# Optimization experiments

Measured on AMD Instinct MI355X. Metric: run time of the kernel, lower is better.

The kernel has to match this reference:

```python
import jax, jax.numpy as jnp
import numpy as np


def _gather_masked(seq, mask, k):
    """Order-preserving gather of the k True positions per row (apply_mask).
    mask rows are constructed to have exactly k ones, so pad_sequence is a no-op."""
    # stable argsort of ~mask puts True-position indices first, in original order
    idx = jnp.argsort(jnp.logical_not(mask), axis=1, stable=True)[:, :k]  # (B, k)
    return jnp.take_along_axis(seq, idx[:, :, None], axis=1)  # (B, k, H)


def setup_inputs() -> dict:
    B, L, H, K = 8, 4096, 1024, 512
    key = jax.random.key(0)
    k1, k2, k3 = jax.random.split(key, 3)
    sequence_output = jax.random.normal(k1, (B, L, H), dtype=jnp.float32)
    # masks: exactly K source and K target positions per sample (disjoint)
    rng = np.random.default_rng(0)
    src_mask = np.zeros((B, L), dtype=bool)
    tgt_mask = np.zeros((B, L), dtype=bool)
    for i in range(B):
        perm = rng.permutation(L)
        src_mask[i, perm[:K]] = True
        tgt_mask[i, perm[K:2 * K]] = True
    weight = jax.random.normal(k2, (2 * H,), dtype=jnp.float32) * 0.02  # classifier Linear(2H -> 1)
    bias = jax.random.normal(k3, (1,), dtype=jnp.float32) * 0.02
    return {
        "sequence_output": sequence_output,
        "source_mask": jnp.asarray(src_mask),
        "target_mask": jnp.asarray(tgt_mask),
        "weight": weight,
        "bias": bias,
        "num_tokens": K,
    }


def reference(sequence_output, source_mask, target_mask, weight, bias, num_tokens):
    B, L, H = sequence_output.shape
    K = num_tokens  # S == T == K (required by the original expand())
    src = _gather_masked(sequence_output, source_mask, K)  # (B, K, H)
    tgt = _gather_masked(sequence_output, target_mask, K)  # (B, K, H)
    # Original: cat([src.unsqueeze(2).expand(B,S,T,H), tgt.unsqueeze(2).expand(B,S,T,H)])
    # -> combined[b,s,t] = [src[b,s], tgt[b,s]]  (target indexed by s, faithful to source)
    # Decompose Linear(2H,1) on the broadcast-concat: col[b,s] = src@w1 + tgt@w2 + b,
    # then broadcast over t. Same math, no (B,S,T,2H) intermediate.
    col = src @ weight[:H] + tgt @ weight[H:] + bias[0]  # (B, K)
    return jnp.broadcast_to(col[:, :, None], (B, K, K))  # logits (B, S, T)
```

## Files before the change

### kernel.cpp

```cpp
#include <hip/hip_runtime.h>
#include <hip/hip_bf16.h>


#define L_DIM 4096
#define H_DIM 1024
#define K_DIM 512
#define B_DIM 8

__global__ __launch_bounds__(64) void compact_kernel(
    const void* __restrict__ src_mask, const void* __restrict__ tgt_mask,
    int* __restrict__ src_idx, int* __restrict__ tgt_idx)
{
    const int w = blockIdx.x;
    const int lane = threadIdx.x;
    const int b = w >> 1;
    const unsigned char* mp = (const unsigned char*)((w & 1) ? tgt_mask : src_mask);
    int* op = ((w & 1) ? tgt_idx : src_idx) + b * K_DIM;

    unsigned long long m = 0ull;
    {
        const uint4* pb = (const uint4*)(mp + (size_t)b * L_DIM);
#pragma unroll
        for (int j = 0; j < 4; ++j) {
            uint4 u = pb[lane * 4 + j];
            const unsigned vals[4] = {u.x, u.y, u.z, u.w};
#pragma unroll
            for (int k = 0; k < 4; ++k) {
                const unsigned v = vals[k];
                const int base = j * 16 + k * 4;
                if (v & 0x000000FFu) m |= 1ull << (base + 0);
                if (v & 0x0000FF00u) m |= 1ull << (base + 1);
                if (v & 0x00FF0000u) m |= 1ull << (base + 2);
                if (v & 0xFF000000u) m |= 1ull << (base + 3);
            }
        }
    }
    int cnt = __popcll(m);
    int tot = cnt;
#pragma unroll
    for (int off = 32; off; off >>= 1) tot += __shfl_xor(tot, off, 64);

    if (tot != K_DIM) {
        m = 0ull;
        const uint4* pi = (const uint4*)((const unsigned*)mp + (size_t)b * L_DIM);
#pragma unroll
        for (int j = 0; j < 16; ++j) {
            uint4 u = pi[lane * 16 + j];
            const int base = j * 4;
            if (u.x) m |= 1ull << (base + 0);
            if (u.y) m |= 1ull << (base + 1);
            if (u.z) m |= 1ull << (base + 2);
            if (u.w) m |= 1ull << (base + 3);
        }
        cnt = __popcll(m);
    }

    int x = cnt;
#pragma unroll
    for (int off = 1; off < 64; off <<= 1) {
        int y = __shfl_up(x, off, 64);
        if (lane >= off) x += y;
    }
    int rank = x - cnt;

    const int basepos = lane * 64;
    while (m) {
        const int j = __builtin_ctzll(m);
        m &= m - 1;
        op[rank++] = basepos + j;
    }
}

__global__ __launch_bounds__(256) void col_bcast_kernel(
    const float* __restrict__ seq, const float* __restrict__ weight,
    const float* __restrict__ bias,
    const int* __restrict__ src_idx, const int* __restrict__ tgt_idx,
    float* __restrict__ out)
{
    const int wave = (blockIdx.x * 256 + threadIdx.x) >> 6;
    const int lane = threadIdx.x & 63;
    const int b = wave >> 9;

    const int ls = src_idx[wave];
    const int lt = tgt_idx[wave];

    const float4* __restrict__ srow = (const float4*)(seq + ((size_t)b * L_DIM + ls) * H_DIM);
    const float4* __restrict__ trow = (const float4*)(seq + ((size_t)b * L_DIM + lt) * H_DIM);
    const float4* __restrict__ w1 = (const float4*)(weight);
    const float4* __restrict__ w2 = (const float4*)(weight + H_DIM);

    float acc0 = 0.f, acc1 = 0.f;
#pragma unroll
    for (int j = 0; j < 4; ++j) {
        const int i = lane + 64 * j;
        float4 a = srow[i], wa = w1[i];
        float4 c = trow[i], wc = w2[i];
        acc0 += a.x * wa.x + a.y * wa.y + a.z * wa.z + a.w * wa.w;
        acc1 += c.x * wc.x + c.y * wc.y + c.z * wc.z + c.w * wc.w;
    }
    float acc = acc0 + acc1;
#pragma unroll
    for (int off = 32; off; off >>= 1) acc += __shfl_xor(acc, off, 64);

    const float col = acc + bias[0];
    const float4 v = make_float4(col, col, col, col);
    float4* __restrict__ orow = (float4*)(out + (size_t)wave * K_DIM);
    orow[lane] = v;
    orow[lane + 64] = v;
}

extern "C" void kernel_launch(void* const* d_in, const int* in_sizes, int n_in,
                              void* d_out, int out_size, void* d_ws, size_t ws_size,
                              hipStream_t stream) {
    const float* seq    = (const float*)d_in[0];
    const void*  smask  = d_in[1];
    const void*  tmask  = d_in[2];
    const float* weight = (const float*)d_in[3];
    const float* bias   = (const float*)d_in[4];
    float* out = (float*)d_out;

    int* ws = (int*)d_ws;
    int* src_idx = ws;
    int* tgt_idx = ws + B_DIM * K_DIM;

    compact_kernel<<<16, 64, 0, stream>>>(smask, tmask, src_idx, tgt_idx);
    col_bcast_kernel<<<(B_DIM * K_DIM) / 4, 256, 0, stream>>>(seq, weight, bias, src_idx, tgt_idx, out);
}
```

Baseline: 16.11 us.

## Fuse mask compaction into dot-product kernel with per-wave nth-set-bit lookup

Removes the separate compaction kernel and its workspace round-trip. Each wave now reads the two 4 KB mask rows for its batch, does a prefix scan of the per-lane popcounts, and finds its own s-th set position with a ballot plus a binary nth-set-bit search. This saves one launch and a dependency, but the mask scan is repeated by all 4096 waves instead of 16. Output stores are also made nontemporal.

```diff
diff --git a/kernel.cpp b/kernel.cpp
--- a/kernel.cpp
+++ b/kernel.cpp
@@ -7,85 +7,89 @@
 #define K_DIM 512
 #define B_DIM 8
 
-__global__ __launch_bounds__(64) void compact_kernel(
-    const void* __restrict__ src_mask, const void* __restrict__ tgt_mask,
-    int* __restrict__ src_idx, int* __restrict__ tgt_idx)
-{
-    const int w = blockIdx.x;
-    const int lane = threadIdx.x;
-    const int b = w >> 1;
-    const unsigned char* mp = (const unsigned char*)((w & 1) ? tgt_mask : src_mask);
-    int* op = ((w & 1) ? tgt_idx : src_idx) + b * K_DIM;
+typedef float f32x4 __attribute__((ext_vector_type(4)));
 
-    unsigned long long m = 0ull;
-    {
-        const uint4* pb = (const uint4*)(mp + (size_t)b * L_DIM);
-#pragma unroll
-        for (int j = 0; j < 4; ++j) {
-            uint4 u = pb[lane * 4 + j];
-            const unsigned vals[4] = {u.x, u.y, u.z, u.w};
-#pragma unroll
-            for (int k = 0; k < 4; ++k) {
-                const unsigned v = vals[k];
-                const int base = j * 16 + k * 4;
-                if (v & 0x000000FFu) m |= 1ull << (base + 0);
-                if (v & 0x0000FF00u) m |= 1ull << (base + 1);
-                if (v & 0x00FF0000u) m |= 1ull << (base + 2);
-                if (v & 0xFF000000u) m |= 1ull << (base + 3);
-            }
-        }
-    }
-    int cnt = __popcll(m);
-    int tot = cnt;
-#pragma unroll
-    for (int off = 32; off; off >>= 1) tot += __shfl_xor(tot, off, 64);
-
-    if (tot != K_DIM) {
-        m = 0ull;
-        const uint4* pi = (const uint4*)((const unsigned*)mp + (size_t)b * L_DIM);
-#pragma unroll
-        for (int j = 0; j < 16; ++j) {
-            uint4 u = pi[lane * 16 + j];
-            const int base = j * 4;
-            if (u.x) m |= 1ull << (base + 0);
-            if (u.y) m |= 1ull << (base + 1);
-            if (u.z) m |= 1ull << (base + 2);
-            if (u.w) m |= 1ull << (base + 3);
-        }
-        cnt = __popcll(m);
-    }
-
-    int x = cnt;
-#pragma unroll
-    for (int off = 1; off < 64; off <<= 1) {
-        int y = __shfl_up(x, off, 64);
-        if (lane >= off) x += y;
-    }
-    int rank = x - cnt;
-
-    const int basepos = lane * 64;
-    while (m) {
-        const int j = __builtin_ctzll(m);
-        m &= m - 1;
-        op[rank++] = basepos + j;
-    }
+__device__ __forceinline__ int nth_set(unsigned long long m, int n) {
+    int pos = 0, c;
+    c = __popcll(m & 0xFFFFFFFFull); if (n >= c) { n -= c; pos += 32; m >>= 32; }
+    c = __popcll(m & 0xFFFFull);     if (n >= c) { n -= c; pos += 16; m >>= 16; }
+    c = __popcll(m & 0xFFull);       if (n >= c) { n -= c; pos += 8;  m >>= 8;  }
+    c = __popcll(m & 0xFull);        if (n >= c) { n -= c; pos += 4;  m >>= 4;  }
+    c = __popcll(m & 0x3ull);        if (n >= c) { n -= c; pos += 2;  m >>= 2;  }
+    c = (int)(m & 1ull);             if (n >= c) { pos += 1; }
+    return pos;
 }
 
-__global__ __launch_bounds__(256) void col_bcast_kernel(
-    const float* __restrict__ seq, const float* __restrict__ weight,
-    const float* __restrict__ bias,
-    const int* __restrict__ src_idx, const int* __restrict__ tgt_idx,
+__global__ __launch_bounds__(256) void fused_kernel(
+    const float* __restrict__ seq,
+    const void* __restrict__ smask, const void* __restrict__ tmask,
+    const float* __restrict__ weight, const float* __restrict__ bias,
     float* __restrict__ out)
 {
     const int wave = (blockIdx.x * 256 + threadIdx.x) >> 6;
     const int lane = threadIdx.x & 63;
     const int b = wave >> 9;
+    const int s = wave & (K_DIM - 1);
 
-    const int ls = src_idx[wave];
-    const int lt = tgt_idx[wave];
+    int pos[2];
+#pragma unroll
+    for (int mi = 0; mi < 2; ++mi) {
+        const unsigned char* mp = (const unsigned char*)(mi ? tmask : smask);
+        unsigned long long m = 0ull;
+        {
+            const uint4* pb = (const uint4*)(mp + (size_t)b * L_DIM);
+#pragma unroll
+            for (int j = 0; j < 4; ++j) {
+                uint4 u = pb[lane * 4 + j];
+                const unsigned vals[4] = {u.x, u.y, u.z, u.w};
+#pragma unroll
+                for (int k = 0; k < 4; ++k) {
+                    const unsigned v = vals[k];
+                    const int base = j * 16 + k * 4;
+                    if (v & 0x000000FFu) m |= 1ull << (base + 0);
+                    if (v & 0x0000FF00u) m |= 1ull << (base + 1);
+                    if (v & 0x00FF0000u) m |= 1ull << (base + 2);
+                    if (v & 0xFF000000u) m |= 1ull << (base + 3);
+                }
+            }
+        }
+        int cnt = __popcll(m);
+        int x = cnt;
+#pragma unroll
+        for (int off = 1; off < 64; off <<= 1) {
+            int y = __shfl_up(x, off, 64);
+            if (lane >= off) x += y;
+        }
+        if (__shfl(x, 63, 64) != K_DIM) {
+            m = 0ull;
+            const uint4* pi = (const uint4*)((const unsigned*)mp + (size_t)b * L_DIM);
+#pragma unroll
+            for (int j = 0; j < 16; ++j) {
+                uint4 u = pi[lane * 16 + j];
+                const int base = j * 4;
+                if (u.x) m |= 1ull << (base + 0);
+                if (u.y) m |= 1ull << (base + 1);
+                if (u.z) m |= 1ull << (base + 2);
+                if (u.w) m |= 1ull << (base + 3);
+            }
+            cnt = __popcll(m);
+            x = cnt;
+#pragma unroll
+            for (int off = 1; off < 64; off <<= 1) {
+                int y = __shfl_up(x, off, 64);
+                if (lane >= off) x += y;
+            }
+        }
+        const int exc = x - cnt;
+        const bool own = (s >= exc) & (s < x);
+        const unsigned long long sel = __ballot(own);
+        const int l = (int)__builtin_ctzll(sel);
+        const int p = own ? (lane * 64 + nth_set(m, s - exc)) : 0;
+        pos[mi] = __shfl(p, l, 64);
+    }
 
-    const float4* __restrict__ srow = (const float4*)(seq + ((size_t)b * L_DIM + ls) * H_DIM);
-    const float4* __restrict__ trow = (const float4*)(seq + ((size_t)b * L_DIM + lt) * H_DIM);
+    const float4* __restrict__ srow = (const float4*)(seq + ((size_t)b * L_DIM + pos[0]) * H_DIM);
+    const float4* __restrict__ trow = (const float4*)(seq + ((size_t)b * L_DIM + pos[1]) * H_DIM);
     const float4* __restrict__ w1 = (const float4*)(weight);
     const float4* __restrict__ w2 = (const float4*)(weight + H_DIM);
 
@@ -103,10 +107,10 @@
     for (int off = 32; off; off >>= 1) acc += __shfl_xor(acc, off, 64);
 
     const float col = acc + bias[0];
-    const float4 v = make_float4(col, col, col, col);
-    float4* __restrict__ orow = (float4*)(out + (size_t)wave * K_DIM);
-    orow[lane] = v;
-    orow[lane + 64] = v;
+    const f32x4 v = {col, col, col, col};
+    f32x4* orow = (f32x4*)(out + (size_t)wave * K_DIM);
+    __builtin_nontemporal_store(v, &orow[lane]);
+    __builtin_nontemporal_store(v, &orow[lane + 64]);
 }
 
 extern "C" void kernel_launch(void* const* d_in, const int* in_sizes, int n_in,
@@ -118,11 +122,7 @@
     const float* weight = (const float*)d_in[3];
     const float* bias   = (const float*)d_in[4];
     float* out = (float*)d_out;
+    (void)d_ws; (void)ws_size;
 
-    int* ws = (int*)d_ws;
-    int* src_idx = ws;
-    int* tgt_idx = ws + B_DIM * K_DIM;
-
-    compact_kernel<<<16, 64, 0, stream>>>(smask, tmask, src_idx, tgt_idx);
-    col_bcast_kernel<<<(B_DIM * K_DIM) / 4, 256, 0, stream>>>(seq, weight, bias, src_idx, tgt_idx, out);
+    fused_kernel<<<(B_DIM * K_DIM) / 4, 256, 0, stream>>>(seq, smask, tmask, weight, bias, out);
 }
```

Measured after the change: 26.64 us. 65.4% more time.
